# Kernel tuning notes

Measured on AMD Instinct MI355X. Metric: run time of the kernel, lower is better.

The kernel has to match this reference:

```python
import jax, jax.numpy as jnp
import numpy as np

N_NODES = 50000
N_EDGES = 800000
GNN_IN, GNN_HID, COMB = 256, 64, 64
MLP_IN, MLP_HID = 256, 512


def glorot(key, shape):
    fan_in, fan_out = shape[0], shape[1]
    s = jnp.sqrt(6.0 / (fan_in + fan_out)).astype(jnp.float32)
    return jax.random.uniform(key, shape, jnp.float32, -s, s)


def setup_inputs() -> dict:
    key = jax.random.key(0)
    ks = jax.random.split(key, 12)
    x = jax.random.normal(ks[0], (N_NODES, GNN_IN), jnp.float32)
    edge_index = jax.random.randint(ks[1], (2, N_EDGES), 0, N_NODES, jnp.int64 if jax.config.jax_enable_x64 else jnp.int32)
    edge_attr = jax.random.uniform(ks[2], (N_EDGES,), jnp.float32)
    user_features = jax.random.normal(ks[3], (N_NODES, MLP_IN), jnp.float32)
    params = {
        'gcn1_W': glorot(ks[4], (GNN_IN, GNN_HID)),
        'gcn1_b': jnp.zeros((GNN_HID,), jnp.float32),
        'gcn2_W': glorot(ks[5], (GNN_HID, COMB)),
        'gcn2_b': jnp.zeros((COMB,), jnp.float32),
        'fc1_W': glorot(ks[6], (MLP_IN, MLP_HID)),
        'fc1_b': jnp.zeros((MLP_HID,), jnp.float32),
        'fc2_W': glorot(ks[7], (MLP_HID, COMB)),
        'fc2_b': jnp.zeros((COMB,), jnp.float32),
        'fcf_W': glorot(ks[8], (2 * COMB, 1)),
        'fcf_b': jnp.zeros((1,), jnp.float32),
    }
    return dict(x=x, edge_index=edge_index, edge_attr=edge_attr,
                user_features=user_features, **params)


def gcn_conv(x, W, b, src, dst, ew, n_nodes):
    # PyG GCNConv: transform, add self-loops (weight 1), sym-normalize, scatter-add.
    h = x @ W  # [N, out]
    loop = jnp.arange(n_nodes, dtype=src.dtype)
    src_sl = jnp.concatenate([src, loop])
    dst_sl = jnp.concatenate([dst, loop])
    ew_sl = jnp.concatenate([ew, jnp.ones((n_nodes,), ew.dtype)])
    deg = jax.ops.segment_sum(ew_sl, dst_sl, num_segments=n_nodes)
    dinv = jnp.where(deg > 0, jax.lax.rsqrt(jnp.maximum(deg, 1e-12)), 0.0)
    norm = dinv[src_sl] * ew_sl * dinv[dst_sl]  # [E+N]
    msg = h[src_sl] * norm[:, None]             # gather + scale
    out = jax.ops.segment_sum(msg, dst_sl, num_segments=n_nodes)
    return out + b


def reference(x, edge_index, edge_attr, user_features,
              gcn1_W, gcn1_b, gcn2_W, gcn2_b,
              fc1_W, fc1_b, fc2_W, fc2_b, fcf_W, fcf_b):
    src, dst = edge_index[0], edge_index[1]
    n = x.shape[0]
    # MLP branch
    mlp_out = jax.nn.relu(user_features @ fc1_W + fc1_b) @ fc2_W + fc2_b
    # GNN branch
    g = gcn_conv(x, gcn1_W, gcn1_b, src, dst, edge_attr, n)
    g = jax.nn.relu(g)
    gnn_out = gcn_conv(g, gcn2_W, gcn2_b, src, dst, edge_attr, n)
    combined = jnp.concatenate([mlp_out, gnn_out], axis=-1)
    return combined @ fcf_W + fcf_b
```

## Files before the change

kernel.cpp:

```cpp
#include <hip/hip_runtime.h>
#include <hip/hip_bf16.h>

#define N_NODES 50000
#define N_EDGES 800000
#define BROW 264

typedef __attribute__((ext_vector_type(8))) short bfrag8;
typedef __attribute__((ext_vector_type(4))) float f32x4;
typedef __attribute__((ext_vector_type(4))) unsigned short us4;
typedef __attribute__((ext_vector_type(8))) unsigned short us8;

__device__ __forceinline__ float bf2f(unsigned short u) {
  return __uint_as_float(((unsigned int)u) << 16);
}
__device__ __forceinline__ unsigned short f2bf(float f) {
  unsigned int u = __float_as_uint(f);
  u = (u + 0x7fffu + ((u >> 16) & 1u)) >> 16;
  return (unsigned short)u;
}
__device__ __forceinline__ float ldS(const void* p, int f32, size_t i) {
  return f32 ? ((const float*)p)[i] : bf2f(((const unsigned short*)p)[i]);
}
__device__ __forceinline__ void stO(void* out, int f32, int i, float v) {
  if (f32) ((float*)out)[i] = v;
  else ((unsigned short*)out)[i] = f2bf(v);
}

template <int F32>
__device__ __forceinline__ void stageB8(const void* src, int nb,
                                        unsigned short* __restrict__ Bs) {
  const int t = threadIdx.x;
  const int r = t >> 3;
  const int q = t & 7;
  int row = nb + r;
  row = row < N_NODES ? row : (N_NODES - 1);
  const size_t base = (size_t)row * 256 + q * 32;
  unsigned short* dst = Bs + r * BROW + q * 32;
  if (F32) {
    const f32x4* s4 = (const f32x4*)((const float*)src + base);
#pragma unroll
    for (int j = 0; j < 4; ++j) {
      f32x4 a = s4[2 * j], b = s4[2 * j + 1];
      us8 o;
      o[0] = f2bf(a[0]); o[1] = f2bf(a[1]); o[2] = f2bf(a[2]); o[3] = f2bf(a[3]);
      o[4] = f2bf(b[0]); o[5] = f2bf(b[1]); o[6] = f2bf(b[2]); o[7] = f2bf(b[3]);
      *(us8*)(dst + j * 8) = o;
    }
  } else {
    const us8* s8 = (const us8*)((const unsigned short*)src + base);
#pragma unroll
    for (int j = 0; j < 4; ++j) *(us8*)(dst + j * 8) = s8[j];
  }
}

__global__ void k_detect(const void* x, const void* ea, const void* uf,
                         const void* f1W, const int* ei, int* flags) {
  int lane = threadIdx.x & 63;
  unsigned short ux = ((const unsigned short*)x)[lane];
  unsigned short ue = ((const unsigned short*)ea)[lane];
  unsigned short uu = ((const unsigned short*)uf)[lane];
  unsigned short uw = ((const unsigned short*)f1W)[lane];
  int oi = ei[2 * lane + 1];
  unsigned long long bx = __ballot(((ux >> 7) & 0xFF) > 0x85);
  unsigned long long be = __ballot((ue & 0x8000u) != 0);
  unsigned long long bu = __ballot(((uu >> 7) & 0xFF) > 0x85);
  unsigned long long bw = __ballot(((uw >> 7) & 0xFF) > 0x7E);
  unsigned long long bi = __ballot(oi != 0);
  if (lane == 0) {
    int fx = bx ? 1 : 0, fe = be ? 1 : 0, fu = bu ? 1 : 0, fw = bw ? 1 : 0;
    flags[0] = fx; flags[1] = fe; flags[2] = fu; flags[3] = fw;
    flags[4] = (bi == 0ull) ? 1 : 0;
    flags[5] = (fx & fe & fu & fw);
  }
}

__global__ __launch_bounds__(256) void k_zeroc(int* __restrict__ counts) {
  int i = blockIdx.x * 256 + threadIdx.x;
  if (i <= N_NODES) counts[i] = 0;
}

__global__ __launch_bounds__(256) void k_histpos(const int* __restrict__ ei,
                                                 const int* __restrict__ flags,
                                                 int* __restrict__ counts,
                                                 int* __restrict__ posw) {
  int e = blockIdx.x * 256 + threadIdx.x;
  if (e >= N_EDGES) return;
  int d;
  if (flags[4]) d = ei[1600000 + 2 * e];
  else          d = ei[800000 + e];
  d = d < 0 ? 0 : (d > N_NODES - 1 ? N_NODES - 1 : d);
  posw[e] = atomicAdd(&counts[d], 1);
}

__global__ __launch_bounds__(256) void k_scan1(const int* __restrict__ cnt,
                                               int* __restrict__ rp,
                                               int* __restrict__ bsum) {
  __shared__ int sd[256];
  int t = threadIdx.x;
  int i0 = blockIdx.x * 1024 + t * 4;
  int v0 = (i0 + 0) < N_NODES ? cnt[i0 + 0] : 0;
  int v1 = (i0 + 1) < N_NODES ? cnt[i0 + 1] : 0;
  int v2 = (i0 + 2) < N_NODES ? cnt[i0 + 2] : 0;
  int v3 = (i0 + 3) < N_NODES ? cnt[i0 + 3] : 0;
  int ts = v0 + v1 + v2 + v3;
  sd[t] = ts;
  __syncthreads();
  for (int off = 1; off < 256; off <<= 1) {
    int x = (t >= off) ? sd[t - off] : 0;
    __syncthreads();
    sd[t] += x;
    __syncthreads();
  }
  int exoff = sd[t] - ts;
  if (i0 + 0 < N_NODES) rp[i0 + 0] = exoff;
  if (i0 + 1 < N_NODES) rp[i0 + 1] = exoff + v0;
  if (i0 + 2 < N_NODES) rp[i0 + 2] = exoff + v0 + v1;
  if (i0 + 3 < N_NODES) rp[i0 + 3] = exoff + v0 + v1 + v2;
  if (t == 255) bsum[blockIdx.x] = sd[255];
}

__global__ void k_scan2(const int* __restrict__ bsum, int* __restrict__ boff,
                        int* __restrict__ rp, int nb) {
  if (threadIdx.x == 0) {
    int run = 0;
    for (int b = 0; b < nb; ++b) { boff[b] = run; run += bsum[b]; }
    rp[N_NODES] = run;
  }
}

__global__ __launch_bounds__(256) void k_scan3(int* __restrict__ rp,
                                               const int* __restrict__ boff) {
  int i = blockIdx.x * 256 + threadIdx.x;
  if (i < N_NODES) rp[i] += boff[i >> 10];
}

__global__ __launch_bounds__(256) void k_placeb(const int* __restrict__ ei,
                                                const void* ea,
                                                const int* __restrict__ flags,
                                                const int* __restrict__ rp,
                                                const int* __restrict__ posw,
                                                unsigned long long* __restrict__ e8) {
  int e = blockIdx.x * 256 + threadIdx.x;
  if (e >= N_EDGES) return;
  int s, d;
  if (flags[4]) { s = ei[2 * e]; d = ei[1600000 + 2 * e]; }
  else          { s = ei[e];     d = ei[800000 + e]; }
  s = s < 0 ? 0 : (s > N_NODES - 1 ? N_NODES - 1 : s);
  d = d < 0 ? 0 : (d > N_NODES - 1 ? N_NODES - 1 : d);
  float w = ldS(ea, flags[1], e);
  int pos = rp[d] + posw[e];
  e8[pos] = ((unsigned long long)__float_as_uint(w) << 32) | (unsigned int)s;
}

__global__ __launch_bounds__(256) void k_degc(const int* __restrict__ rp,
                                              const unsigned long long* __restrict__ e8,
                                              float* __restrict__ dinv) {
  const int i = blockIdx.x * 4 + (threadIdx.x >> 6);
  if (i >= N_NODES) return;
  const int lane = threadIdx.x & 63;
  const int base = rp[i], end = rp[i + 1];
  float s = 0.f;
  for (int j = base + lane; j < end; j += 64)
    s += __uint_as_float((unsigned int)(e8[j] >> 32));
#pragma unroll
  for (int off = 32; off > 0; off >>= 1) s += __shfl_xor(s, off, 64);
  if (lane == 0) dinv[i] = rsqrtf(s + 1.0f);
}

__global__ __launch_bounds__(512) void k_prep(
    const void* f1W, const void* g1W, const void* f2W, const void* f2b,
    const void* g2W, const void* g2b, const void* ffW, const void* ffb,
    const int* __restrict__ flags, unsigned short* __restrict__ W1T,
    unsigned short* __restrict__ WgT, float* __restrict__ w2f,
    float* __restrict__ w2g, float* __restrict__ constv) {
  const int fw = flags[3];
  if (blockIdx.x < 288) {
    int tid = blockIdx.x * 512 + threadIdx.x;
    if (tid < 512 * 256) {
      int c = tid >> 8, k = tid & 255;
      W1T[tid] = f2bf(ldS(f1W, fw, (size_t)k * 512 + c));
    } else if (tid < 512 * 256 + 64 * 256) {
      int j = tid - 512 * 256;
      int c = j >> 8, k = j & 255;
      WgT[j] = f2bf(ldS(g1W, fw, (size_t)k * 64 + c));
    }
    return;
  }
  int t = threadIdx.x;
  if (t < 512) {
    float s = 0.f;
    for (int c = 0; c < 64; ++c) s += ldS(f2W, fw, t * 64 + c) * ldS(ffW, fw, c);
    w2f[t] = s;
  }
  if (t < 64) {
    float s = 0.f;
    for (int c = 0; c < 64; ++c) s += ldS(g2W, fw, t * 64 + c) * ldS(ffW, fw, 64 + c);
    w2g[t] = s;
  }
  if (t == 0) {
    float s = ldS(ffb, fw, 0);
    for (int c = 0; c < 64; ++c) {
      s += ldS(f2b, fw, c) * ldS(ffW, fw, c);
      s += ldS(g2b, fw, c) * ldS(ffW, fw, 64 + c);
    }
    constv[0] = s;
  }
}

__global__ __launch_bounds__(512, 2) void k_h13u(
    const void* x, const unsigned short* __restrict__ WgT,
    const float* __restrict__ dinv, const int* __restrict__ flags,
    unsigned short* __restrict__ h1b) {
  __shared__ __align__(16) unsigned short Bs[64 * BROW];
  const int nb = blockIdx.x * 64;
  if (flags[0]) stageB8<1>(x, nb, Bs);
  else          stageB8<0>(x, nb, Bs);
  __syncthreads();

  const int lane = threadIdx.x & 63;
  const int wave = threadIdx.x >> 6;
  const int ct = wave & 3;
  const int nh = wave >> 2;
  const int l15 = lane & 15;
  const int quad = lane >> 4;
  const unsigned short* ap = WgT + (size_t)(ct * 16 + l15) * 256 + quad * 8;

  f32x4 acc[2];
  acc[0] = (f32x4){0.f, 0.f, 0.f, 0.f};
  acc[1] = (f32x4){0.f, 0.f, 0.f, 0.f};

#pragma unroll
  for (int ks = 0; ks < 8; ++ks) {
    bfrag8 a = *(const bfrag8*)(ap + ks * 32);
    const int bofs = ks * 32 + quad * 8;
#pragma unroll
    for (int u = 0; u < 2; ++u) {
      bfrag8 b = *(const bfrag8*)(Bs + (nh * 32 + u * 16 + l15) * BROW + bofs);
      acc[u] = __builtin_amdgcn_mfma_f32_16x16x32_bf16(a, b, acc[u], 0, 0, 0);
    }
  }
#pragma unroll
  for (int u = 0; u < 2; ++u) {
    int node = nb + nh * 32 + u * 16 + l15;
    if (node < N_NODES) {
      float di = dinv[node];
      us4 o;
#pragma unroll
      for (int r = 0; r < 4; ++r) o[r] = f2bf(acc[u][r] * di);
      *(us4*)(h1b + (size_t)node * 64 + ct * 16 + quad * 4) = o;
    }
  }
}

__global__ __launch_bounds__(512, 2) void k_mlpu(
    const void* uf, const unsigned short* __restrict__ W1T,
    const void* fc1b, const float* __restrict__ w2f,
    const int* __restrict__ flags, float* __restrict__ mlpc) {
  __shared__ __align__(16) unsigned short Bs[64 * BROW];
  const int nb = blockIdx.x * 64;
  if (flags[2]) stageB8<1>(uf, nb, Bs);
  else          stageB8<0>(uf, nb, Bs);
  __syncthreads();

  const int fw = flags[3];
  const int lane = threadIdx.x & 63;
  const int wave = threadIdx.x >> 6;
  const int l15 = lane & 15;
  const int quad = lane >> 4;
  const int c_base = wave * 64;
  const unsigned short* ap = W1T + (size_t)(c_base + l15) * 256 + quad * 8;

  f32x4 acc[4][4];
#pragma unroll
  for (int t = 0; t < 4; ++t)
#pragma unroll
    for (int u = 0; u < 4; ++u) acc[t][u] = (f32x4){0.f, 0.f, 0.f, 0.f};

#pragma unroll
  for (int ks = 0; ks < 8; ++ks) {
    const int bofs = ks * 32 + quad * 8;
    bfrag8 b[4];
#pragma unroll
    for (int u = 0; u < 4; ++u)
      b[u] = *(const bfrag8*)(Bs + (u * 16 + l15) * BROW + bofs);
#pragma unroll
    for (int t = 0; t < 4; ++t) {
      bfrag8 a = *(const bfrag8*)(ap + (size_t)t * 16 * 256 + ks * 32);
#pragma unroll
      for (int u = 0; u < 4; ++u)
        acc[t][u] = __builtin_amdgcn_mfma_f32_16x16x32_bf16(a, b[u], acc[t][u], 0, 0, 0);
    }
  }
  __syncthreads();

  float part[4] = {0.f, 0.f, 0.f, 0.f};
#pragma unroll
  for (int t = 0; t < 4; ++t) {
#pragma unroll
    for (int r = 0; r < 4; ++r) {
      const int c = c_base + t * 16 + quad * 4 + r;
      const float bc = ldS(fc1b, fw, c);
      const float wc = w2f[c];
#pragma unroll
      for (int u = 0; u < 4; ++u) {
        float v = acc[t][u][r] + bc;
        v = v > 0.f ? v : 0.f;
        part[u] += v * wc;
      }
    }
  }
  float* red = (float*)Bs;
#pragma unroll
  for (int u = 0; u < 4; ++u) {
    part[u] += __shfl_xor(part[u], 16, 64);
    part[u] += __shfl_xor(part[u], 32, 64);
    if (lane < 16) red[wave * 64 + u * 16 + l15] = part[u];
  }
  __syncthreads();
  const int t = threadIdx.x;
  if (t < 64) {
    float sum = 0.f;
#pragma unroll
    for (int w = 0; w < 8; ++w) sum += red[w * 64 + t];
    int node = nb + t;
    if (node < N_NODES) mlpc[node] = sum;
  }
}

__global__ __launch_bounds__(256) void k_aggs2(
    const int* __restrict__ rp, const unsigned long long* __restrict__ e8,
    const unsigned short* __restrict__ h1b, const float* __restrict__ dinv,
    const void* g1b, const float* __restrict__ w2g,
    const int* __restrict__ flags, float* __restrict__ s2) {
  const int i = blockIdx.x * 4 + (threadIdx.x >> 6);
  if (i >= N_NODES) return;
  const int lane = threadIdx.x & 63;
  const int base = rp[i], end = rp[i + 1];
  const float di = dinv[i];
  float acc = 0.f;
  int j = base;
  for (; j + 8 <= end; j += 8) {
    unsigned long long vv[8];
#pragma unroll
    for (int q = 0; q < 8; ++q) vv[q] = e8[j + q];
    float ww[8], hv[8];
#pragma unroll
    for (int q = 0; q < 8; ++q) {
      ww[q] = __uint_as_float((unsigned int)(vv[q] >> 32));
      hv[q] = bf2f(h1b[(size_t)(unsigned int)vv[q] * 64 + lane]);
    }
#pragma unroll
    for (int q = 0; q < 8; ++q) acc += ww[q] * hv[q];
  }
  for (; j < end; ++j) {
    unsigned long long v = e8[j];
    acc += __uint_as_float((unsigned int)(v >> 32)) *
           bf2f(h1b[(size_t)(unsigned int)v * 64 + lane]);
  }
  float v = (acc + bf2f(h1b[(size_t)i * 64 + lane])) * di + ldS(g1b, flags[3], lane);
  v = v > 0.f ? v : 0.f;
  float p = v * w2g[lane];
#pragma unroll
  for (int off = 32; off > 0; off >>= 1) p += __shfl_xor(p, off, 64);
  if (lane == 0) s2[i] = di * p;
}

__global__ __launch_bounds__(256) void k_fin2(
    const int* __restrict__ rp, const unsigned long long* __restrict__ e8,
    const float* __restrict__ s2, const float* __restrict__ dinv,
    const float* __restrict__ mlpc, const float* __restrict__ constv,
    const int* __restrict__ flags, void* out) {
  const int i = blockIdx.x * 4 + (threadIdx.x >> 6);
  if (i >= N_NODES) return;
  const int lane = threadIdx.x & 63;
  const int base = rp[i], end = rp[i + 1];
  float p = 0.f;
  for (int j = base + lane; j < end; j += 64) {
    unsigned long long v = e8[j];
    p += __uint_as_float((unsigned int)(v >> 32)) * s2[(unsigned int)v];
  }
#pragma unroll
  for (int off = 32; off > 0; off >>= 1) p += __shfl_xor(p, off, 64);
  if (lane == 0) {
    float di = dinv[i];
    stO(out, flags[5], i, mlpc[i] + di * (p + s2[i]) + constv[0]);
  }
}

__global__ __launch_bounds__(256) void k_zero(const int* __restrict__ flags, void* out) {
  int i = blockIdx.x * 256 + threadIdx.x;
  if (i < N_NODES) stO(out, flags[5], i, 0.f);
}

extern "C" void kernel_launch(void* const* d_in, const int* in_sizes, int n_in,
                              void* d_out, int out_size, void* d_ws, size_t ws_size,
                              hipStream_t stream) {
  const void* x   = d_in[0];
  const int*  ei  = (const int*)d_in[1];
  const void* ea  = d_in[2];
  const void* uf  = d_in[3];
  const void* g1W = d_in[4];
  const void* g1b = d_in[5];
  const void* g2W = d_in[6];
  const void* g2b = d_in[7];
  const void* f1W = d_in[8];
  const void* f1b = d_in[9];
  const void* f2W = d_in[10];
  const void* f2b = d_in[11];
  const void* ffW = d_in[12];
  const void* ffb = d_in[13];

  float* ws = (float*)d_ws;
  int*   flags  = (int*)ws;
  float* w2f    = ws + 16;
  float* w2g    = ws + 528;
  float* constv = ws + 592;
  float* dinv   = ws + 608;
  float* s2     = ws + 50608;
  float* mlpc   = ws + 100608;
  unsigned short* W1T = (unsigned short*)(ws + 150608);
  unsigned short* WgT = W1T + 131072;
  int* rowptr = (int*)(ws + 224336);
  int* bsum   = (int*)(ws + 274352);
  int* boff   = bsum + 64;
  int* counts = (int*)(ws + 274480);
  int* posw   = (int*)(ws + 324496);
  unsigned long long* e8 = (unsigned long long*)(ws + 1124496);
  unsigned short* h1b = (unsigned short*)(ws + 2724496);
  const size_t NEED = (size_t)4324496 * 4;

  k_detect<<<1, 64, 0, stream>>>(x, ea, uf, f1W, ei, flags);
  if (ws_size < NEED) {
    k_zero<<<(N_NODES + 255) / 256, 256, 0, stream>>>(flags, d_out);
    return;
  }
  const int NZB = (N_NODES + 256) / 256;
  const int NB  = (N_NODES + 1023) / 1024;
  const int NGB = (N_NODES + 63) / 64;
  const int NEB = (N_EDGES + 255) / 256;

  k_zeroc<<<NZB, 256, 0, stream>>>(counts);
  k_histpos<<<NEB, 256, 0, stream>>>(ei, flags, counts, posw);
  k_scan1<<<NB, 256, 0, stream>>>(counts, rowptr, bsum);
  k_scan2<<<1, 64, 0, stream>>>(bsum, boff, rowptr, NB);
  k_scan3<<<(N_NODES + 255) / 256, 256, 0, stream>>>(rowptr, boff);
  k_placeb<<<NEB, 256, 0, stream>>>(ei, ea, flags, rowptr, posw, e8);
  k_degc<<<(N_NODES + 3) / 4, 256, 0, stream>>>(rowptr, e8, dinv);
  k_prep<<<289, 512, 0, stream>>>(f1W, g1W, f2W, f2b, g2W, g2b, ffW, ffb, flags,
                                  W1T, WgT, w2f, w2g, constv);
  k_h13u<<<NGB, 512, 0, stream>>>(x, WgT, dinv, flags, h1b);
  k_mlpu<<<NGB, 512, 0, stream>>>(uf, W1T, f1b, w2f, flags, mlpc);
  k_aggs2<<<(N_NODES + 3) / 4, 256, 0, stream>>>(rowptr, e8, h1b, dinv, g1b, w2g, flags, s2);
  k_fin2<<<(N_NODES + 3) / 4, 256, 0, stream>>>(rowptr, e8, s2, dinv, mlpc, constv, flags, d_out);
}
```

Baseline: 360.3 us.

## Make dense GEMM kernels persistent with register-cached weights and double-buffered staging

The h1 projection and MLP kernels become persistent grids (512 and 256 blocks) that loop over 64-node tiles. Each block loads its weight fragments into registers once and double-buffers the input tile in shared memory, prefetching the next tile's bf16 data into registers while MFMAs run on the current one. The staging thread mapping also changes to row-major-by-lane. This aims to cut repeated weight loads and hide global load latency, at the cost of more registers and LDS (two buffers), which may lower occupancy, and fewer blocks in flight.

```diff
diff --git a/kernel.cpp b/kernel.cpp
--- a/kernel.cpp
+++ b/kernel.cpp
@@ -4,6 +4,9 @@
 #define N_NODES 50000
 #define N_EDGES 800000
 #define BROW 264
+#define NT_TILES 782
+#define GRID_MLP 256
+#define GRID_H13 512
 
 typedef __attribute__((ext_vector_type(8))) short bfrag8;
 typedef __attribute__((ext_vector_type(4))) float f32x4;
@@ -26,30 +29,35 @@
   else ((unsigned short*)out)[i] = f2bf(v);
 }
 
-template <int F32>
-__device__ __forceinline__ void stageB8(const void* src, int nb,
-                                        unsigned short* __restrict__ Bs) {
+__device__ __forceinline__ void stageLoadBF(const void* src, int nb, us8 st[4]) {
   const int t = threadIdx.x;
-  const int r = t >> 3;
-  const int q = t & 7;
-  int row = nb + r;
-  row = row < N_NODES ? row : (N_NODES - 1);
-  const size_t base = (size_t)row * 256 + q * 32;
+  const int r = t & 63, q = t >> 6;
+  int row = nb + r; row = row < N_NODES ? row : (N_NODES - 1);
+  const us8* s8 = (const us8*)((const unsigned short*)src + (size_t)row * 256 + q * 32);
+#pragma unroll
+  for (int j = 0; j < 4; ++j) st[j] = s8[j];
+}
+__device__ __forceinline__ void stageWrite(const us8 st[4], unsigned short* __restrict__ Bs) {
+  const int t = threadIdx.x;
+  const int r = t & 63, q = t >> 6;
   unsigned short* dst = Bs + r * BROW + q * 32;
-  if (F32) {
-    const f32x4* s4 = (const f32x4*)((const float*)src + base);
-#pragma unroll
-    for (int j = 0; j < 4; ++j) {
-      f32x4 a = s4[2 * j], b = s4[2 * j + 1];
-      us8 o;
-      o[0] = f2bf(a[0]); o[1] = f2bf(a[1]); o[2] = f2bf(a[2]); o[3] = f2bf(a[3]);
-      o[4] = f2bf(b[0]); o[5] = f2bf(b[1]); o[6] = f2bf(b[2]); o[7] = f2bf(b[3]);
-      *(us8*)(dst + j * 8) = o;
-    }
-  } else {
-    const us8* s8 = (const us8*)((const unsigned short*)src + base);
-#pragma unroll
-    for (int j = 0; j < 4; ++j) *(us8*)(dst + j * 8) = s8[j];
+#pragma unroll
+  for (int j = 0; j < 4; ++j) *(us8*)(dst + j * 8) = st[j];
+}
+__device__ __forceinline__ void stageF32(const void* src, int nb,
+                                         unsigned short* __restrict__ Bs) {
+  const int t = threadIdx.x;
+  const int r = t & 63, q = t >> 6;
+  int row = nb + r; row = row < N_NODES ? row : (N_NODES - 1);
+  const f32x4* s4 = (const f32x4*)((const float*)src + (size_t)row * 256 + q * 32);
+  unsigned short* dst = Bs + r * BROW + q * 32;
+#pragma unroll
+  for (int j = 0; j < 4; ++j) {
+    f32x4 a = s4[2 * j], b = s4[2 * j + 1];
+    us8 o;
+    o[0] = f2bf(a[0]); o[1] = f2bf(a[1]); o[2] = f2bf(a[2]); o[3] = f2bf(a[3]);
+    o[4] = f2bf(b[0]); o[5] = f2bf(b[1]); o[6] = f2bf(b[2]); o[7] = f2bf(b[3]);
+    *(us8*)(dst + j * 8) = o;
   }
 }
 
@@ -207,123 +215,167 @@
   }
 }
 
-__global__ __launch_bounds__(512, 2) void k_h13u(
+__global__ __launch_bounds__(512, 2) void k_h13P(
     const void* x, const unsigned short* __restrict__ WgT,
     const float* __restrict__ dinv, const int* __restrict__ flags,
     unsigned short* __restrict__ h1b) {
-  __shared__ __align__(16) unsigned short Bs[64 * BROW];
-  const int nb = blockIdx.x * 64;
-  if (flags[0]) stageB8<1>(x, nb, Bs);
-  else          stageB8<0>(x, nb, Bs);
-  __syncthreads();
-
+  __shared__ __align__(16) unsigned short Bs[2][64 * BROW];
+  const int f32in = flags[0];
   const int lane = threadIdx.x & 63;
   const int wave = threadIdx.x >> 6;
   const int ct = wave & 3;
   const int nh = wave >> 2;
   const int l15 = lane & 15;
   const int quad = lane >> 4;
-  const unsigned short* ap = WgT + (size_t)(ct * 16 + l15) * 256 + quad * 8;
-
-  f32x4 acc[2];
-  acc[0] = (f32x4){0.f, 0.f, 0.f, 0.f};
-  acc[1] = (f32x4){0.f, 0.f, 0.f, 0.f};
-
-#pragma unroll
-  for (int ks = 0; ks < 8; ++ks) {
-    bfrag8 a = *(const bfrag8*)(ap + ks * 32);
-    const int bofs = ks * 32 + quad * 8;
+
+  bfrag8 A[8];
+  {
+    const unsigned short* ap = WgT + (size_t)(ct * 16 + l15) * 256 + quad * 8;
+#pragma unroll
+    for (int ks = 0; ks < 8; ++ks) A[ks] = *(const bfrag8*)(ap + ks * 32);
+  }
+
+  int tile = blockIdx.x;
+  if (f32in) stageF32(x, tile * 64, Bs[0]);
+  else { us8 st[4]; stageLoadBF(x, tile * 64, st); stageWrite(st, Bs[0]); }
+  __syncthreads();
+
+  int cur = 0;
+  for (; tile < NT_TILES; tile += GRID_H13) {
+    const int nxt = tile + GRID_H13;
+    const bool have = nxt < NT_TILES;
+    us8 st[4];
+    if (!f32in && have) stageLoadBF(x, nxt * 64, st);
+
+    f32x4 acc[2];
+    acc[0] = (f32x4){0.f, 0.f, 0.f, 0.f};
+    acc[1] = (f32x4){0.f, 0.f, 0.f, 0.f};
+    const unsigned short* Bc = Bs[cur];
+#pragma unroll
+    for (int ks = 0; ks < 8; ++ks) {
+      const int bofs = ks * 32 + quad * 8;
+#pragma unroll
+      for (int u = 0; u < 2; ++u) {
+        bfrag8 b = *(const bfrag8*)(Bc + (nh * 32 + u * 16 + l15) * BROW + bofs);
+        acc[u] = __builtin_amdgcn_mfma_f32_16x16x32_bf16(A[ks], b, acc[u], 0, 0, 0);
+      }
+    }
+
+    if (have) {
+      if (f32in) stageF32(x, nxt * 64, Bs[cur ^ 1]);
+      else       stageWrite(st, Bs[cur ^ 1]);
+    }
+
 #pragma unroll
     for (int u = 0; u < 2; ++u) {
-      bfrag8 b = *(const bfrag8*)(Bs + (nh * 32 + u * 16 + l15) * BROW + bofs);
-      acc[u] = __builtin_amdgcn_mfma_f32_16x16x32_bf16(a, b, acc[u], 0, 0, 0);
-    }
-  }
-#pragma unroll
-  for (int u = 0; u < 2; ++u) {
-    int node = nb + nh * 32 + u * 16 + l15;
-    if (node < N_NODES) {
-      float di = dinv[node];
-      us4 o;
-#pragma unroll
-      for (int r = 0; r < 4; ++r) o[r] = f2bf(acc[u][r] * di);
-      *(us4*)(h1b + (size_t)node * 64 + ct * 16 + quad * 4) = o;
-    }
-  }
-}
-
-__global__ __launch_bounds__(512, 2) void k_mlpu(
+      int node = tile * 64 + nh * 32 + u * 16 + l15;
+      if (node < N_NODES) {
+        float di = dinv[node];
+        us4 o;
+#pragma unroll
+        for (int r = 0; r < 4; ++r) o[r] = f2bf(acc[u][r] * di);
+        *(us4*)(h1b + (size_t)node * 64 + ct * 16 + quad * 4) = o;
+      }
+    }
+    __syncthreads();
+    cur ^= 1;
+  }
+}
+
+__global__ __launch_bounds__(512, 2) void k_mlpP(
     const void* uf, const unsigned short* __restrict__ W1T,
     const void* fc1b, const float* __restrict__ w2f,
     const int* __restrict__ flags, float* __restrict__ mlpc) {
-  __shared__ __align__(16) unsigned short Bs[64 * BROW];
-  const int nb = blockIdx.x * 64;
-  if (flags[2]) stageB8<1>(uf, nb, Bs);
-  else          stageB8<0>(uf, nb, Bs);
-  __syncthreads();
-
+  __shared__ __align__(16) unsigned short Bs[2][64 * BROW];
+  __shared__ float red[2][512];
+  const int f32in = flags[2];
   const int fw = flags[3];
   const int lane = threadIdx.x & 63;
   const int wave = threadIdx.x >> 6;
   const int l15 = lane & 15;
   const int quad = lane >> 4;
   const int c_base = wave * 64;
-  const unsigned short* ap = W1T + (size_t)(c_base + l15) * 256 + quad * 8;
-
-  f32x4 acc[4][4];
-#pragma unroll
-  for (int t = 0; t < 4; ++t)
-#pragma unroll
-    for (int u = 0; u < 4; ++u) acc[t][u] = (f32x4){0.f, 0.f, 0.f, 0.f};
-
-#pragma unroll
-  for (int ks = 0; ks < 8; ++ks) {
-    const int bofs = ks * 32 + quad * 8;
-    bfrag8 b[4];
-#pragma unroll
-    for (int u = 0; u < 4; ++u)
-      b[u] = *(const bfrag8*)(Bs + (u * 16 + l15) * BROW + bofs);
+
+  bfrag8 A[4][8];
+  {
+    const unsigned short* ap = W1T + (size_t)(c_base + l15) * 256 + quad * 8;
+#pragma unroll
+    for (int t = 0; t < 4; ++t)
+#pragma unroll
+      for (int ks = 0; ks < 8; ++ks)
+        A[t][ks] = *(const bfrag8*)(ap + (size_t)t * 16 * 256 + ks * 32);
+  }
+
+  int tile = blockIdx.x;
+  if (f32in) stageF32(uf, tile * 64, Bs[0]);
+  else { us8 st[4]; stageLoadBF(uf, tile * 64, st); stageWrite(st, Bs[0]); }
+  __syncthreads();
+
+  int cur = 0, pp = 0;
+  for (; tile < NT_TILES; tile += GRID_MLP) {
+    const int nxt = tile + GRID_MLP;
+    const bool have = nxt < NT_TILES;
+    us8 st[4];
+    if (!f32in && have) stageLoadBF(uf, nxt * 64, st);
+
+    f32x4 acc[4][4];
+#pragma unroll
+    for (int t = 0; t < 4; ++t)
+#pragma unroll
+      for (int u = 0; u < 4; ++u) acc[t][u] = (f32x4){0.f, 0.f, 0.f, 0.f};
+
+    const unsigned short* Bc = Bs[cur];
+#pragma unroll
+    for (int ks = 0; ks < 8; ++ks) {
+      const int bofs = ks * 32 + quad * 8;
+      bfrag8 b[4];
+#pragma unroll
+      for (int u = 0; u < 4; ++u)
+        b[u] = *(const bfrag8*)(Bc + (u * 16 + l15) * BROW + bofs);
+#pragma unroll
+      for (int t = 0; t < 4; ++t)
+#pragma unroll
+        for (int u = 0; u < 4; ++u)
+          acc[t][u] = __builtin_amdgcn_mfma_f32_16x16x32_bf16(A[t][ks], b[u], acc[t][u], 0, 0, 0);
+    }
+
+    float part[4] = {0.f, 0.f, 0.f, 0.f};
 #pragma unroll
     for (int t = 0; t < 4; ++t) {
-      bfrag8 a = *(const bfrag8*)(ap + (size_t)t * 16 * 256 + ks * 32);
-#pragma unroll
-      for (int u = 0; u < 4; ++u)
-        acc[t][u] = __builtin_amdgcn_mfma_f32_16x16x32_bf16(a, b[u], acc[t][u], 0, 0, 0);
-    }
-  }
-  __syncthreads();
-
-  float part[4] = {0.f, 0.f, 0.f, 0.f};
-#pragma unroll
-  for (int t = 0; t < 4; ++t) {
-#pragma unroll
-    for (int r = 0; r < 4; ++r) {
-      const int c = c_base + t * 16 + quad * 4 + r;
-      const float bc = ldS(fc1b, fw, c);
-      const float wc = w2f[c];
-#pragma unroll
-      for (int u = 0; u < 4; ++u) {
-        float v = acc[t][u][r] + bc;
-        v = v > 0.f ? v : 0.f;
-        part[u] += v * wc;
+#pragma unroll
+      for (int r = 0; r < 4; ++r) {
+        const int c = c_base + t * 16 + quad * 4 + r;
+        const float bc = ldS(fc1b, fw, c);
+        const float wc = w2f[c];
+#pragma unroll
+        for (int u = 0; u < 4; ++u) {
+          float v = acc[t][u][r] + bc;
+          v = v > 0.f ? v : 0.f;
+          part[u] += v * wc;
+        }
       }
     }
-  }
-  float* red = (float*)Bs;
-#pragma unroll
-  for (int u = 0; u < 4; ++u) {
-    part[u] += __shfl_xor(part[u], 16, 64);
-    part[u] += __shfl_xor(part[u], 32, 64);
-    if (lane < 16) red[wave * 64 + u * 16 + l15] = part[u];
-  }
-  __syncthreads();
-  const int t = threadIdx.x;
-  if (t < 64) {
-    float sum = 0.f;
-#pragma unroll
-    for (int w = 0; w < 8; ++w) sum += red[w * 64 + t];
-    int node = nb + t;
-    if (node < N_NODES) mlpc[node] = sum;
+
+    if (have) {
+      if (f32in) stageF32(uf, nxt * 64, Bs[cur ^ 1]);
+      else       stageWrite(st, Bs[cur ^ 1]);
+    }
+
+#pragma unroll
+    for (int u = 0; u < 4; ++u) {
+      part[u] += __shfl_xor(part[u], 16, 64);
+      part[u] += __shfl_xor(part[u], 32, 64);
+      if (lane < 16) red[pp][wave * 64 + u * 16 + l15] = part[u];
+    }
+    __syncthreads();
+    if (threadIdx.x < 64) {
+      float sum = 0.f;
+#pragma unroll
+      for (int w = 0; w < 8; ++w) sum += red[pp][w * 64 + threadIdx.x];
+      int node = tile * 64 + threadIdx.x;
+      if (node < N_NODES) mlpc[node] = sum;
+    }
+    cur ^= 1; pp ^= 1;
   }
 }
 
@@ -436,7 +488,6 @@
   }
   const int NZB = (N_NODES + 256) / 256;
   const int NB  = (N_NODES + 1023) / 1024;
-  const int NGB = (N_NODES + 63) / 64;
   const int NEB = (N_EDGES + 255) / 256;
 
   k_zeroc<<<NZB, 256, 0, stream>>>(counts);
@@ -448,8 +499,8 @@
   k_degc<<<(N_NODES + 3) / 4, 256, 0, stream>>>(rowptr, e8, dinv);
   k_prep<<<289, 512, 0, stream>>>(f1W, g1W, f2W, f2b, g2W, g2b, ffW, ffb, flags,
                                   W1T, WgT, w2f, w2g, constv);
-  k_h13u<<<NGB, 512, 0, stream>>>(x, WgT, dinv, flags, h1b);
-  k_mlpu<<<NGB, 512, 0, stream>>>(uf, W1T, f1b, w2f, flags, mlpc);
+  k_h13P<<<GRID_H13, 512, 0, stream>>>(x, WgT, dinv, flags, h1b);
+  k_mlpP<<<GRID_MLP, 512, 0, stream>>>(uf, W1T, f1b, w2f, flags, mlpc);
   k_aggs2<<<(N_NODES + 3) / 4, 256, 0, stream>>>(rowptr, e8, h1b, dinv, g1b, w2g, flags, s2);
   k_fin2<<<(N_NODES + 3) / 4, 256, 0, stream>>>(rowptr, e8, s2, dinv, mlpc, constv, flags, d_out);
 }
```

After: 352.3 us. 1.02x faster.
